# Kernel optimization log

Hardware: AMD Instinct MI355X
Metric: run time of the kernel (lower is better)

Reference implementation:

```python
import jax, jax.numpy as jnp
import numpy as np

N_UE = 100000
N_AP = 10000
N_E = 1600000
D = 64
H = 128


def setup_inputs() -> dict:
    key = jax.random.key(0)
    ks = jax.random.split(key, 10)
    s = 0.05
    return {
        "ue_hid": jax.random.normal(ks[0], (N_UE, D), jnp.float32),
        "ap_hid": jax.random.normal(ks[1], (N_AP, D), jnp.float32),
        "edge_hid": jax.random.normal(ks[2], (N_E, D), jnp.float32),
        "src": jax.random.randint(ks[3], (N_E,), 0, N_UE),
        "dst": jax.random.randint(ks[4], (N_E,), 0, N_AP),
        "W1a": jax.random.normal(ks[5], (2 * D, H), jnp.float32) * s,
        "b1a": jnp.zeros((H,), jnp.float32),
        "W1b": jax.random.normal(ks[6], (H, H), jnp.float32) * s,
        "b1b": jnp.zeros((H,), jnp.float32),
        "W2a": jax.random.normal(ks[7], (D + H, H), jnp.float32) * s,
        "b2a": jnp.zeros((H,), jnp.float32),
        "W2b": jax.random.normal(ks[8], (H, D), jnp.float32) * s,
        "b2b": jnp.zeros((D,), jnp.float32),
    }


def reference(ue_hid, ap_hid, edge_hid, src, dst,
              W1a, b1a, W1b, b1b, W2a, b2a, W2b, b2b):
    # message: concat(edge_feature, src UE feature) -> [E, 2D]
    msg = jnp.concatenate([edge_hid, ue_hid[src]], axis=-1)
    # mlp1 applied per edge (DGL applies it inside reduce on the mailbox,
    # which is equivalent to per-edge application followed by segment sum)
    h = jnp.maximum(msg @ W1a + b1a, 0.0) @ W1b + b1b          # [E, H]
    # sum over mailbox (all edges with the same destination AP)
    agg = jax.ops.segment_sum(h, dst, num_segments=N_AP)        # [N_AP, H]
    # mlp2 on concat(AP hid, aggregated messages)
    z = jnp.concatenate([ap_hid, agg], axis=-1)                 # [N_AP, D+H]
    new_ap = jnp.maximum(z @ W2a + b2a, 0.0) @ W2b + b2b        # [N_AP, D]
    return new_ap
```

## Files before the change

### kernel.cpp

```cpp
#include <hip/hip_runtime.h>
#include <hip/hip_bf16.h>

#define N_UE 100000
#define N_AP 10000
#define N_E  1600000
#define DD   64
#define HH   128
#define NTILE (N_E / 128)

typedef float f32x4 __attribute__((ext_vector_type(4)));
typedef short s8b   __attribute__((ext_vector_type(8)));
typedef short s4b   __attribute__((ext_vector_type(4)));

static __device__ __forceinline__ unsigned short f2bf(float x) {
  union { float f; unsigned int u; } v; v.f = x;
  unsigned int r = v.u + 0x7fffu + ((v.u >> 16) & 1u);
  return (unsigned short)(r >> 16);
}

__global__ void apk0_prep(const float* __restrict__ W1a, short* __restrict__ WTg,
                          int* __restrict__ counts, float* __restrict__ aggW) {
  int i = blockIdx.x * 256 + threadIdx.x;
  int n = gridDim.x * 256;
  for (int x = i; x < 128 * 128; x += n) {
    int col = x >> 7, k = x & 127;
    WTg[x] = (short)f2bf(W1a[k * 128 + col]);
  }
  for (int x = i; x < N_AP; x += n) counts[x] = 0;
  for (int x = i; x < N_AP * 128 / 4; x += n)
    ((float4*)aggW)[x] = make_float4(0.f, 0.f, 0.f, 0.f);
}

__global__ void apk2_hist(const int* __restrict__ dst, int* __restrict__ counts) {
  int i = blockIdx.x * blockDim.x + threadIdx.x;
  int stride = gridDim.x * blockDim.x;
  for (; i < N_E; i += stride) atomicAdd(&counts[dst[i]], 1);
}

__global__ __launch_bounds__(256) void apk3_scan(const int* __restrict__ counts,
                                                 int* __restrict__ offsets,
                                                 int* __restrict__ cursor) {
  __shared__ int p[256];
  int t = threadIdx.x;
  const int CH = 40;
  int start = t * CH, end = min(start + CH, N_AP);
  int s = 0;
  for (int i = start; i < end; i++) s += counts[i];
  p[t] = s;
  __syncthreads();
  for (int d = 1; d < 256; d <<= 1) {
    int v = p[t] + ((t >= d) ? p[t - d] : 0);
    __syncthreads();
    p[t] = v;
    __syncthreads();
  }
  int base = (t == 0) ? 0 : p[t - 1];
  for (int i = start; i < end; i++) {
    offsets[i] = base;
    cursor[i] = base;
    base += counts[i];
  }
  if (t == 255) offsets[N_AP] = base;
}

__global__ void apk4_scatter(const int* __restrict__ dst, const int* __restrict__ src,
                             int* __restrict__ cursor, int4* __restrict__ triple) {
  int i = blockIdx.x * blockDim.x + threadIdx.x;
  int stride = gridDim.x * blockDim.x;
  for (; i < N_E; i += stride) {
    int d = dst[i];
    int pos = atomicAdd(&cursor[d], 1);
    triple[pos] = make_int4(i, src[i], d, 0);
  }
}

__global__ __launch_bounds__(256, 4) void apk5_edges(
    const float* __restrict__ edge_hid, const float* __restrict__ ue_hid,
    const short* __restrict__ WTg, const float* __restrict__ b1a,
    const int4* __restrict__ triple, float* __restrict__ aggW) {
  __shared__ short A[128][132];
  __shared__ int segs[128];
  int t = threadIdx.x;
  int wave = t >> 6, lane = t & 63, quad = lane >> 4, l16 = lane & 15;

  s8b bf[2][4];
  for (int ct = 0; ct < 2; ct++)
    for (int ks = 0; ks < 4; ks++)
      bf[ct][ks] = *(const s8b*)&WTg[(wave * 32 + ct * 16 + l16) * 128 +
                                     ks * 32 + quad * 8];
  float bias0 = b1a[wave * 32 + l16];
  float bias1 = b1a[wave * 32 + 16 + l16];

  int runseg = -1;
  float run0 = 0.f, run1 = 0.f;
  auto flush = [&]() {
    if (runseg >= 0) {
      float f0 = run0 + __shfl_xor(run0, 16); f0 += __shfl_xor(f0, 32);
      float f1 = run1 + __shfl_xor(run1, 16); f1 += __shfl_xor(f1, 32);
      if (quad == 0) {
        atomicAdd(&aggW[(size_t)runseg * 128 + wave * 32 + l16], f0);
        atomicAdd(&aggW[(size_t)runseg * 128 + wave * 32 + 16 + l16], f1);
      }
    }
  };

  const int r = t >> 1, h = t & 1;
  for (int tile = blockIdx.x; tile < NTILE; tile += gridDim.x) {
    int4 tr = triple[(size_t)tile * 128 + r];
    __syncthreads();
    if (h == 0) segs[r] = tr.z;
    {
      const float* srow = h ? (ue_hid + (size_t)tr.y * 64)
                            : (edge_hid + (size_t)tr.x * 64);
      int kb = h * 64;
      #pragma unroll
      for (int cc = 0; cc < 8; cc++) {
        float4 v = ((const float4*)srow)[cc * 2];
        float4 w = ((const float4*)srow)[cc * 2 + 1];
        s8b p;
        p[0] = (short)f2bf(v.x); p[1] = (short)f2bf(v.y);
        p[2] = (short)f2bf(v.z); p[3] = (short)f2bf(v.w);
        p[4] = (short)f2bf(w.x); p[5] = (short)f2bf(w.y);
        p[6] = (short)f2bf(w.z); p[7] = (short)f2bf(w.w);
        *(s8b*)&A[r][kb + cc * 8] = p;
      }
    }
    __syncthreads();

    for (int rt = 0; rt < 8; rt++) {
      s8b a0 = *(const s8b*)&A[rt * 16 + l16][0 + quad * 8];
      s8b a1 = *(const s8b*)&A[rt * 16 + l16][32 + quad * 8];
      s8b a2 = *(const s8b*)&A[rt * 16 + l16][64 + quad * 8];
      s8b a3 = *(const s8b*)&A[rt * 16 + l16][96 + quad * 8];
      f32x4 c0 = {0.f, 0.f, 0.f, 0.f}, c1 = {0.f, 0.f, 0.f, 0.f};
      c0 = __builtin_amdgcn_mfma_f32_16x16x32_bf16(a0, bf[0][0], c0, 0, 0, 0);
      c0 = __builtin_amdgcn_mfma_f32_16x16x32_bf16(a1, bf[0][1], c0, 0, 0, 0);
      c0 = __builtin_amdgcn_mfma_f32_16x16x32_bf16(a2, bf[0][2], c0, 0, 0, 0);
      c0 = __builtin_amdgcn_mfma_f32_16x16x32_bf16(a3, bf[0][3], c0, 0, 0, 0);
      c1 = __builtin_amdgcn_mfma_f32_16x16x32_bf16(a0, bf[1][0], c1, 0, 0, 0);
      c1 = __builtin_amdgcn_mfma_f32_16x16x32_bf16(a1, bf[1][1], c1, 0, 0, 0);
      c1 = __builtin_amdgcn_mfma_f32_16x16x32_bf16(a2, bf[1][2], c1, 0, 0, 0);
      c1 = __builtin_amdgcn_mfma_f32_16x16x32_bf16(a3, bf[1][3], c1, 0, 0, 0);
      float t0[4], t1[4];
      #pragma unroll
      for (int j = 0; j < 4; j++) {
        t0[j] = fmaxf(c0[j] + bias0, 0.f);
        t1[j] = fmaxf(c1[j] + bias1, 0.f);
      }
      int gb = rt * 16;
      int sF = segs[gb], sL = segs[gb + 15];
      if (sF == sL) {
        if (sF != runseg) { flush(); runseg = sF; run0 = 0.f; run1 = 0.f; }
        run0 += t0[0] + t0[1] + t0[2] + t0[3];
        run1 += t1[0] + t1[1] + t1[2] + t1[3];
      } else {
        int sj[4];
        #pragma unroll
        for (int j = 0; j < 4; j++) sj[j] = segs[gb + quad * 4 + j];
        for (int s = sF; s <= sL; s++) {
          float v0 = 0.f, v1 = 0.f;
          #pragma unroll
          for (int j = 0; j < 4; j++)
            if (sj[j] == s) { v0 += t0[j]; v1 += t1[j]; }
          if (s == runseg) { run0 += v0; run1 += v1; }
          else { flush(); runseg = s; run0 = v0; run1 = v1; }
        }
      }
    }
  }
  flush();
}

__global__ __launch_bounds__(256) void apk6_mlp2(
    const float* __restrict__ ap_hid, const float* __restrict__ W1b,
    const float* __restrict__ b1b, const float* __restrict__ W2a,
    const float* __restrict__ b2a, const float* __restrict__ W2b,
    const float* __restrict__ b2b, const float* __restrict__ aggW,
    const int* __restrict__ offsets, float* __restrict__ out) {
  __shared__ float wbuf[64 * 128];
  __shared__ float zrows[16 * 128];
  __shared__ float yrows[16 * 128];
  __shared__ float arows[16 * 64];
  __shared__ float cbuf[16];
  int t = threadIdx.x;
  int apb = blockIdx.x * 16;
  for (int i = t; i < 16 * 128 / 4; i += 256)
    ((float4*)zrows)[i] = ((const float4*)(aggW + (size_t)apb * 128))[i];
  for (int i = t; i < 16 * 64 / 4; i += 256)
    ((float4*)arows)[i] = ((const float4*)(ap_hid + (size_t)apb * 64))[i];
  if (t < 16) cbuf[t] = (float)(offsets[apb + t + 1] - offsets[apb + t]);
  int j = t & 127, half = t >> 7;
  {
    float bb = b1b[j];
    __syncthreads();
    float acc[8];
    for (int r = 0; r < 8; r++) acc[r] = cbuf[half * 8 + r] * bb;
    for (int p = 0; p < 2; p++) {
      __syncthreads();
      for (int i = t; i < 64 * 128 / 4; i += 256)
        ((float4*)wbuf)[i] = ((const float4*)(W1b + p * 64 * 128))[i];
      __syncthreads();
      for (int k = 0; k < 64; k++) {
        float w = wbuf[k * 128 + j];
        for (int r = 0; r < 8; r++)
          acc[r] += zrows[(half * 8 + r) * 128 + (p * 64 + k)] * w;
      }
    }
    for (int r = 0; r < 8; r++) yrows[(half * 8 + r) * 128 + j] = acc[r];
  }
  {
    float acc2[8];
    float bb = b2a[j];
    for (int r = 0; r < 8; r++) acc2[r] = bb;
    __syncthreads();
    for (int i = t; i < 64 * 128 / 4; i += 256)
      ((float4*)wbuf)[i] = ((const float4*)W2a)[i];
    __syncthreads();
    for (int k = 0; k < 64; k++) {
      float w = wbuf[k * 128 + j];
      for (int r = 0; r < 8; r++) acc2[r] += arows[(half * 8 + r) * 64 + k] * w;
    }
    for (int p = 0; p < 2; p++) {
      __syncthreads();
      for (int i = t; i < 64 * 128 / 4; i += 256)
        ((float4*)wbuf)[i] = ((const float4*)(W2a + (64 + p * 64) * 128))[i];
      __syncthreads();
      for (int k = 0; k < 64; k++) {
        float w = wbuf[k * 128 + j];
        for (int r = 0; r < 8; r++)
          acc2[r] += yrows[(half * 8 + r) * 128 + (p * 64 + k)] * w;
      }
    }
    __syncthreads();
    for (int r = 0; r < 8; r++)
      zrows[(half * 8 + r) * 128 + j] = fmaxf(acc2[r], 0.f);
  }
  {
    __syncthreads();
    for (int i = t; i < 128 * 64 / 4; i += 256)
      ((float4*)wbuf)[i] = ((const float4*)W2b)[i];
    __syncthreads();
    int i2 = t & 63, q = t >> 6;
    float acc3[4];
    float bb = b2b[i2];
    for (int r = 0; r < 4; r++) acc3[r] = bb;
    for (int k = 0; k < 128; k++) {
      float w = wbuf[k * 64 + i2];
      for (int r = 0; r < 4; r++) acc3[r] += zrows[(q * 4 + r) * 128 + k] * w;
    }
    for (int r = 0; r < 4; r++)
      out[(size_t)(apb + q * 4 + r) * 64 + i2] = acc3[r];
  }
}

extern "C" void kernel_launch(void* const* d_in, const int* in_sizes, int n_in,
                              void* d_out, int out_size, void* d_ws, size_t ws_size,
                              hipStream_t stream) {
  const float* ue_hid   = (const float*)d_in[0];
  const float* ap_hid   = (const float*)d_in[1];
  const float* edge_hid = (const float*)d_in[2];
  const int*   src      = (const int*)d_in[3];
  const int*   dst      = (const int*)d_in[4];
  const float* W1a      = (const float*)d_in[5];
  const float* b1a      = (const float*)d_in[6];
  const float* W1b      = (const float*)d_in[7];
  const float* b1b      = (const float*)d_in[8];
  const float* W2a      = (const float*)d_in[9];
  const float* b2a      = (const float*)d_in[10];
  const float* W2b      = (const float*)d_in[11];
  const float* b2b      = (const float*)d_in[12];
  float* out = (float*)d_out;

  unsigned char* ws = (unsigned char*)d_ws;
  short* WTg    = (short*)(ws);
  int* counts   = (int*)(ws + 32768);
  int* offsets  = (int*)(ws + 73728);
  int* cursor   = (int*)(ws + 114688);
  float* aggW   = (float*)(ws + 155648);
  int4* triple  = (int4*)(ws + 5275648);

  apk0_prep<<<640, 256, 0, stream>>>(W1a, WTg, counts, aggW);
  apk2_hist<<<2048, 256, 0, stream>>>(dst, counts);
  apk3_scan<<<1, 256, 0, stream>>>(counts, offsets, cursor);
  apk4_scatter<<<2048, 256, 0, stream>>>(dst, src, cursor, triple);
  apk5_edges<<<2048, 256, 0, stream>>>(edge_hid, ue_hid, WTg, b1a, triple, aggW);
  apk6_mlp2<<<N_AP / 16, 256, 0, stream>>>(ap_hid, W1b, b1b, W2a, b2a, W2b, b2b,
                                           aggW, offsets, out);
}
```

Baseline: 917.3 us.

## Fuse preprocessing and edge phases into one cooperative kernel with packed edge records

New measurement: 1.614 ms. 1.76x slower.

```diff
diff --git a/kernel.cpp b/kernel.cpp
--- a/kernel.cpp
+++ b/kernel.cpp
@@ -1,16 +1,17 @@
 #include <hip/hip_runtime.h>
-#include <hip/hip_bf16.h>
+#include <hip/hip_cooperative_groups.h>
+
+namespace cg = cooperative_groups;
 
 #define N_UE 100000
 #define N_AP 10000
 #define N_E  1600000
-#define DD   64
-#define HH   128
 #define NTILE (N_E / 128)
+#define GRID  1024
 
 typedef float f32x4 __attribute__((ext_vector_type(4)));
+typedef int   i32x2 __attribute__((ext_vector_type(2)));
 typedef short s8b   __attribute__((ext_vector_type(8)));
-typedef short s4b   __attribute__((ext_vector_type(4)));
 
 static __device__ __forceinline__ unsigned short f2bf(float x) {
   union { float f; unsigned int u; } v; v.f = x;
@@ -18,68 +19,72 @@
   return (unsigned short)(r >> 16);
 }
 
-__global__ void apk0_prep(const float* __restrict__ W1a, short* __restrict__ WTg,
-                          int* __restrict__ counts, float* __restrict__ aggW) {
-  int i = blockIdx.x * 256 + threadIdx.x;
-  int n = gridDim.x * 256;
+
+static __device__ __forceinline__ void ph0_prep(const float* __restrict__ W1a,
+    short* __restrict__ WTg, int* __restrict__ counts, float* __restrict__ aggW) {
+  int i = blockIdx.x * 256 + threadIdx.x, n = gridDim.x * 256;
   for (int x = i; x < 128 * 128; x += n) {
     int col = x >> 7, k = x & 127;
     WTg[x] = (short)f2bf(W1a[k * 128 + col]);
   }
   for (int x = i; x < N_AP; x += n) counts[x] = 0;
   for (int x = i; x < N_AP * 128 / 4; x += n)
-    ((float4*)aggW)[x] = make_float4(0.f, 0.f, 0.f, 0.f);
-}
-
-__global__ void apk2_hist(const int* __restrict__ dst, int* __restrict__ counts) {
-  int i = blockIdx.x * blockDim.x + threadIdx.x;
-  int stride = gridDim.x * blockDim.x;
-  for (; i < N_E; i += stride) atomicAdd(&counts[dst[i]], 1);
-}
-
-__global__ __launch_bounds__(256) void apk3_scan(const int* __restrict__ counts,
-                                                 int* __restrict__ offsets,
-                                                 int* __restrict__ cursor) {
-  __shared__ int p[256];
-  int t = threadIdx.x;
-  const int CH = 40;
-  int start = t * CH, end = min(start + CH, N_AP);
-  int s = 0;
-  for (int i = start; i < end; i++) s += counts[i];
-  p[t] = s;
+    ((f32x4*)aggW)[x] = (f32x4){0.f, 0.f, 0.f, 0.f};
+}
+
+static __device__ __forceinline__ void ph1_hist(const int* __restrict__ dst,
+                                                int* __restrict__ counts) {
+  int i = blockIdx.x * 256 + threadIdx.x, n = gridDim.x * 256;
+  for (; i < N_E; i += n) atomicAdd(&counts[dst[i]], 1);
+}
+
+static __device__ __forceinline__ void ph2_scanlocal(const int* __restrict__ counts,
+    int* __restrict__ offsets, int* __restrict__ bsum, int* p) {
+  if (blockIdx.x >= 40) return;
+  int t = threadIdx.x, idx = blockIdx.x * 256 + t;
+  int v = (idx < N_AP) ? counts[idx] : 0;
+  p[t] = v;
   __syncthreads();
   for (int d = 1; d < 256; d <<= 1) {
-    int v = p[t] + ((t >= d) ? p[t - d] : 0);
-    __syncthreads();
-    p[t] = v;
-    __syncthreads();
-  }
-  int base = (t == 0) ? 0 : p[t - 1];
-  for (int i = start; i < end; i++) {
-    offsets[i] = base;
-    cursor[i] = base;
-    base += counts[i];
-  }
-  if (t == 255) offsets[N_AP] = base;
-}
-
-__global__ void apk4_scatter(const int* __restrict__ dst, const int* __restrict__ src,
-                             int* __restrict__ cursor, int4* __restrict__ triple) {
-  int i = blockIdx.x * blockDim.x + threadIdx.x;
-  int stride = gridDim.x * blockDim.x;
-  for (; i < N_E; i += stride) {
-    int d = dst[i];
-    int pos = atomicAdd(&cursor[d], 1);
-    triple[pos] = make_int4(i, src[i], d, 0);
-  }
-}
-
-__global__ __launch_bounds__(256, 4) void apk5_edges(
-    const float* __restrict__ edge_hid, const float* __restrict__ ue_hid,
-    const short* __restrict__ WTg, const float* __restrict__ b1a,
-    const int4* __restrict__ triple, float* __restrict__ aggW) {
-  __shared__ short A[128][132];
-  __shared__ int segs[128];
+    int s2 = p[t] + ((t >= d) ? p[t - d] : 0);
+    __syncthreads();
+    p[t] = s2;
+    __syncthreads();
+  }
+  if (idx < N_AP) offsets[idx] = p[t] - v;
+  if (t == 255) bsum[blockIdx.x] = p[255];
+}
+
+static __device__ __forceinline__ void ph3_scanbase(int* __restrict__ offsets,
+    const int* __restrict__ bsum, int* p) {
+  if (blockIdx.x >= 40) return;
+  int t = threadIdx.x, idx = blockIdx.x * 256 + t;
+  if (t == 0) {
+    int b = 0;
+    for (int k = 0; k < (int)blockIdx.x; k++) b += bsum[k];
+    p[0] = b;
+  }
+  __syncthreads();
+  if (idx < N_AP) offsets[idx] += p[0];
+}
+
+static __device__ __forceinline__ void ph4_scatter(const int* __restrict__ dst,
+    const int* __restrict__ src, int* __restrict__ offsets, i32x2* __restrict__ pair) {
+  int i = blockIdx.x * 256 + threadIdx.x, n = gridDim.x * 256;
+  for (; i < N_E; i += n) {
+    int d = dst[i], s = src[i];
+    int pos = atomicAdd(&offsets[d], 1);
+    i32x2 v;
+    v[0] = i | ((d & 0x7FF) << 21);
+    v[1] = s | ((d >> 11) << 17);
+    __builtin_nontemporal_store(v, &pair[pos]);
+  }
+}
+
+static __device__ void ph5_edges(const float* __restrict__ edge_hid,
+    const float* __restrict__ ue_hid, const short* __restrict__ WTg,
+    const float* __restrict__ b1a, const i32x2* __restrict__ pair,
+    float* __restrict__ aggW, short (*A)[132], int* segs) {
   int t = threadIdx.x;
   int wave = t >> 6, lane = t & 63, quad = lane >> 4, l16 = lane & 15;
 
@@ -106,23 +111,37 @@
 
   const int r = t >> 1, h = t & 1;
   for (int tile = blockIdx.x; tile < NTILE; tile += gridDim.x) {
-    int4 tr = triple[(size_t)tile * 128 + r];
-    __syncthreads();
-    if (h == 0) segs[r] = tr.z;
-    {
-      const float* srow = h ? (ue_hid + (size_t)tr.y * 64)
-                            : (edge_hid + (size_t)tr.x * 64);
-      int kb = h * 64;
+    i32x2 tr = __builtin_nontemporal_load(&pair[(size_t)tile * 128 + r]);
+    int e = tr[0] & 0x1FFFFF;
+    int d = (int)((unsigned)tr[0] >> 21) | (((tr[1] >> 17) & 7) << 11);
+    int s = tr[1] & 0x1FFFF;
+    __syncthreads();
+    if (h == 0) {
+      segs[r] = d;
+      const f32x4* s4 = (const f32x4*)(edge_hid + (size_t)e * 64);
       #pragma unroll
       for (int cc = 0; cc < 8; cc++) {
-        float4 v = ((const float4*)srow)[cc * 2];
-        float4 w = ((const float4*)srow)[cc * 2 + 1];
-        s8b p;
-        p[0] = (short)f2bf(v.x); p[1] = (short)f2bf(v.y);
-        p[2] = (short)f2bf(v.z); p[3] = (short)f2bf(v.w);
-        p[4] = (short)f2bf(w.x); p[5] = (short)f2bf(w.y);
-        p[6] = (short)f2bf(w.z); p[7] = (short)f2bf(w.w);
-        *(s8b*)&A[r][kb + cc * 8] = p;
+        f32x4 v = __builtin_nontemporal_load(&s4[cc * 2]);
+        f32x4 w = __builtin_nontemporal_load(&s4[cc * 2 + 1]);
+        s8b pk;
+        pk[0] = (short)f2bf(v[0]); pk[1] = (short)f2bf(v[1]);
+        pk[2] = (short)f2bf(v[2]); pk[3] = (short)f2bf(v[3]);
+        pk[4] = (short)f2bf(w[0]); pk[5] = (short)f2bf(w[1]);
+        pk[6] = (short)f2bf(w[2]); pk[7] = (short)f2bf(w[3]);
+        *(s8b*)&A[r][cc * 8] = pk;
+      }
+    } else {
+      const f32x4* s4 = (const f32x4*)(ue_hid + (size_t)s * 64);
+      #pragma unroll
+      for (int cc = 0; cc < 8; cc++) {
+        f32x4 v = s4[cc * 2];
+        f32x4 w = s4[cc * 2 + 1];
+        s8b pk;
+        pk[0] = (short)f2bf(v[0]); pk[1] = (short)f2bf(v[1]);
+        pk[2] = (short)f2bf(v[2]); pk[3] = (short)f2bf(v[3]);
+        pk[4] = (short)f2bf(w[0]); pk[5] = (short)f2bf(w[1]);
+        pk[6] = (short)f2bf(w[2]); pk[7] = (short)f2bf(w[3]);
+        *(s8b*)&A[r][64 + cc * 8] = pk;
       }
     }
     __syncthreads();
@@ -157,18 +176,56 @@
         int sj[4];
         #pragma unroll
         for (int j = 0; j < 4; j++) sj[j] = segs[gb + quad * 4 + j];
-        for (int s = sF; s <= sL; s++) {
+        for (int sg = sF; sg <= sL; sg++) {
           float v0 = 0.f, v1 = 0.f;
           #pragma unroll
           for (int j = 0; j < 4; j++)
-            if (sj[j] == s) { v0 += t0[j]; v1 += t1[j]; }
-          if (s == runseg) { run0 += v0; run1 += v1; }
-          else { flush(); runseg = s; run0 = v0; run1 = v1; }
+            if (sj[j] == sg) { v0 += t0[j]; v1 += t1[j]; }
+          if (sg == runseg) { run0 += v0; run1 += v1; }
+          else { flush(); runseg = sg; run0 = v0; run1 = v1; }
         }
       }
     }
   }
   flush();
+}
+
+
+__global__ __launch_bounds__(256, 4) void apc_all(
+    const float* __restrict__ W1a, const float* __restrict__ b1a,
+    const float* __restrict__ edge_hid, const float* __restrict__ ue_hid,
+    const int* __restrict__ src, const int* __restrict__ dst,
+    short* __restrict__ WTg, int* __restrict__ counts, int* __restrict__ offsets,
+    int* __restrict__ bsum, i32x2* __restrict__ pair, float* __restrict__ aggW) {
+  __shared__ short A[128][132];
+  __shared__ int segs[128];
+  __shared__ int p[256];
+  cg::grid_group g = cg::this_grid();
+  ph0_prep(W1a, WTg, counts, aggW);          g.sync();
+  ph1_hist(dst, counts);                     g.sync();
+  ph2_scanlocal(counts, offsets, bsum, p);   g.sync();
+  ph3_scanbase(offsets, bsum, p);            g.sync();
+  ph4_scatter(dst, src, offsets, pair);      g.sync();
+  ph5_edges(edge_hid, ue_hid, WTg, b1a, pair, aggW, A, segs);
+}
+
+__global__ __launch_bounds__(256, 4) void apc_one(int phase,
+    const float* __restrict__ W1a, const float* __restrict__ b1a,
+    const float* __restrict__ edge_hid, const float* __restrict__ ue_hid,
+    const int* __restrict__ src, const int* __restrict__ dst,
+    short* __restrict__ WTg, int* __restrict__ counts, int* __restrict__ offsets,
+    int* __restrict__ bsum, i32x2* __restrict__ pair, float* __restrict__ aggW) {
+  __shared__ short A[128][132];
+  __shared__ int segs[128];
+  __shared__ int p[256];
+  switch (phase) {
+    case 0: ph0_prep(W1a, WTg, counts, aggW); break;
+    case 1: ph1_hist(dst, counts); break;
+    case 2: ph2_scanlocal(counts, offsets, bsum, p); break;
+    case 3: ph3_scanbase(offsets, bsum, p); break;
+    case 4: ph4_scatter(dst, src, offsets, pair); break;
+    case 5: ph5_edges(edge_hid, ue_hid, WTg, b1a, pair, aggW, A, segs); break;
+  }
 }
 
 __global__ __launch_bounds__(256) void apk6_mlp2(
@@ -176,7 +233,7 @@
     const float* __restrict__ b1b, const float* __restrict__ W2a,
     const float* __restrict__ b2a, const float* __restrict__ W2b,
     const float* __restrict__ b2b, const float* __restrict__ aggW,
-    const int* __restrict__ offsets, float* __restrict__ out) {
+    const int* __restrict__ counts, float* __restrict__ out) {
   __shared__ float wbuf[64 * 128];
   __shared__ float zrows[16 * 128];
   __shared__ float yrows[16 * 128];
@@ -188,22 +245,22 @@
     ((float4*)zrows)[i] = ((const float4*)(aggW + (size_t)apb * 128))[i];
   for (int i = t; i < 16 * 64 / 4; i += 256)
     ((float4*)arows)[i] = ((const float4*)(ap_hid + (size_t)apb * 64))[i];
-  if (t < 16) cbuf[t] = (float)(offsets[apb + t + 1] - offsets[apb + t]);
+  if (t < 16) cbuf[t] = (float)counts[apb + t];
   int j = t & 127, half = t >> 7;
   {
     float bb = b1b[j];
     __syncthreads();
     float acc[8];
     for (int r = 0; r < 8; r++) acc[r] = cbuf[half * 8 + r] * bb;
-    for (int p = 0; p < 2; p++) {
+    for (int pp = 0; pp < 2; pp++) {
       __syncthreads();
       for (int i = t; i < 64 * 128 / 4; i += 256)
-        ((float4*)wbuf)[i] = ((const float4*)(W1b + p * 64 * 128))[i];
+        ((float4*)wbuf)[i] = ((const float4*)(W1b + pp * 64 * 128))[i];
       __syncthreads();
       for (int k = 0; k < 64; k++) {
         float w = wbuf[k * 128 + j];
         for (int r = 0; r < 8; r++)
-          acc[r] += zrows[(half * 8 + r) * 128 + (p * 64 + k)] * w;
+          acc[r] += zrows[(half * 8 + r) * 128 + (pp * 64 + k)] * w;
       }
     }
     for (int r = 0; r < 8; r++) yrows[(half * 8 + r) * 128 + j] = acc[r];
@@ -220,15 +277,15 @@
       float w = wbuf[k * 128 + j];
       for (int r = 0; r < 8; r++) acc2[r] += arows[(half * 8 + r) * 64 + k] * w;
     }
-    for (int p = 0; p < 2; p++) {
+    for (int pp = 0; pp < 2; pp++) {
       __syncthreads();
       for (int i = t; i < 64 * 128 / 4; i += 256)
-        ((float4*)wbuf)[i] = ((const float4*)(W2a + (64 + p * 64) * 128))[i];
+        ((float4*)wbuf)[i] = ((const float4*)(W2a + (64 + pp * 64) * 128))[i];
       __syncthreads();
       for (int k = 0; k < 64; k++) {
         float w = wbuf[k * 128 + j];
         for (int r = 0; r < 8; r++)
-          acc2[r] += yrows[(half * 8 + r) * 128 + (p * 64 + k)] * w;
+          acc2[r] += yrows[(half * 8 + r) * 128 + (pp * 64 + k)] * w;
       }
     }
     __syncthreads();
@@ -275,15 +332,20 @@
   short* WTg    = (short*)(ws);
   int* counts   = (int*)(ws + 32768);
   int* offsets  = (int*)(ws + 73728);
-  int* cursor   = (int*)(ws + 114688);
-  float* aggW   = (float*)(ws + 155648);
-  int4* triple  = (int4*)(ws + 5275648);
-
-  apk0_prep<<<640, 256, 0, stream>>>(W1a, WTg, counts, aggW);
-  apk2_hist<<<2048, 256, 0, stream>>>(dst, counts);
-  apk3_scan<<<1, 256, 0, stream>>>(counts, offsets, cursor);
-  apk4_scatter<<<2048, 256, 0, stream>>>(dst, src, cursor, triple);
-  apk5_edges<<<2048, 256, 0, stream>>>(edge_hid, ue_hid, WTg, b1a, triple, aggW);
+  int* bsum     = (int*)(ws + 114688);
+  float* aggW   = (float*)(ws + 118784);
+  i32x2* pair   = (i32x2*)(ws + 5238784);
+
+  void* args[] = {(void*)&W1a, (void*)&b1a, (void*)&edge_hid, (void*)&ue_hid,
+                  (void*)&src, (void*)&dst, (void*)&WTg, (void*)&counts,
+                  (void*)&offsets, (void*)&bsum, (void*)&pair, (void*)&aggW};
+  hipError_t cerr = hipLaunchCooperativeKernel((void*)apc_all, dim3(GRID), dim3(256),
+                                               args, 0, stream);
+  if (cerr != hipSuccess) {
+    for (int p = 0; p < 6; p++)
+      apc_one<<<GRID, 256, 0, stream>>>(p, W1a, b1a, edge_hid, ue_hid, src, dst,
+                                        WTg, counts, offsets, bsum, pair, aggW);
+  }
   apk6_mlp2<<<N_AP / 16, 256, 0, stream>>>(ap_hid, W1b, b1b, W2a, b2a, W2b, b2b,
-                                           aggW, offsets, out);
-}
+                                           aggW, counts, out);
+}
```

## Pack edge triples into 8-byte pairs, parallelize scan, coalesce row gathers

Applied to the files above, without the earlier changes.

Result: faster. 829.0 us (-9.6%).

```diff
diff --git a/kernel.cpp b/kernel.cpp
--- a/kernel.cpp
+++ b/kernel.cpp
@@ -1,14 +1,12 @@
 #include <hip/hip_runtime.h>
-#include <hip/hip_bf16.h>
 
 #define N_UE 100000
 #define N_AP 10000
 #define N_E  1600000
-#define DD   64
-#define HH   128
 #define NTILE (N_E / 128)
 
 typedef float f32x4 __attribute__((ext_vector_type(4)));
+typedef int   i32x2 __attribute__((ext_vector_type(2)));
 typedef short s8b   __attribute__((ext_vector_type(8)));
 typedef short s4b   __attribute__((ext_vector_type(4)));
 
@@ -20,15 +18,14 @@
 
 __global__ void apk0_prep(const float* __restrict__ W1a, short* __restrict__ WTg,
                           int* __restrict__ counts, float* __restrict__ aggW) {
-  int i = blockIdx.x * 256 + threadIdx.x;
-  int n = gridDim.x * 256;
+  int i = blockIdx.x * 256 + threadIdx.x, n = gridDim.x * 256;
   for (int x = i; x < 128 * 128; x += n) {
     int col = x >> 7, k = x & 127;
     WTg[x] = (short)f2bf(W1a[k * 128 + col]);
   }
   for (int x = i; x < N_AP; x += n) counts[x] = 0;
   for (int x = i; x < N_AP * 128 / 4; x += n)
-    ((float4*)aggW)[x] = make_float4(0.f, 0.f, 0.f, 0.f);
+    ((f32x4*)aggW)[x] = (f32x4){0.f, 0.f, 0.f, 0.f};
 }
 
 __global__ void apk2_hist(const int* __restrict__ dst, int* __restrict__ counts) {
@@ -37,49 +34,59 @@
   for (; i < N_E; i += stride) atomicAdd(&counts[dst[i]], 1);
 }
 
-__global__ __launch_bounds__(256) void apk3_scan(const int* __restrict__ counts,
-                                                 int* __restrict__ offsets,
-                                                 int* __restrict__ cursor) {
+__global__ __launch_bounds__(256) void apk3a_scanlocal(
+    const int* __restrict__ counts, int* __restrict__ offsets,
+    int* __restrict__ bsum) {
   __shared__ int p[256];
-  int t = threadIdx.x;
-  const int CH = 40;
-  int start = t * CH, end = min(start + CH, N_AP);
-  int s = 0;
-  for (int i = start; i < end; i++) s += counts[i];
-  p[t] = s;
+  int t = threadIdx.x, idx = blockIdx.x * 256 + t;
+  int v = (idx < N_AP) ? counts[idx] : 0;
+  p[t] = v;
   __syncthreads();
   for (int d = 1; d < 256; d <<= 1) {
-    int v = p[t] + ((t >= d) ? p[t - d] : 0);
-    __syncthreads();
-    p[t] = v;
-    __syncthreads();
-  }
-  int base = (t == 0) ? 0 : p[t - 1];
-  for (int i = start; i < end; i++) {
-    offsets[i] = base;
-    cursor[i] = base;
-    base += counts[i];
-  }
-  if (t == 255) offsets[N_AP] = base;
+    int s2 = p[t] + ((t >= d) ? p[t - d] : 0);
+    __syncthreads();
+    p[t] = s2;
+    __syncthreads();
+  }
+  if (idx < N_AP) offsets[idx] = p[t] - v;
+  if (t == 255) bsum[blockIdx.x] = p[255];
+}
+
+__global__ __launch_bounds__(256) void apk3b_scanbase(
+    int* __restrict__ offsets, const int* __restrict__ bsum) {
+  __shared__ int base;
+  int t = threadIdx.x, idx = blockIdx.x * 256 + t;
+  if (t == 0) {
+    int b = 0;
+    for (int k = 0; k < (int)blockIdx.x; k++) b += bsum[k];
+    base = b;
+  }
+  __syncthreads();
+  if (idx < N_AP) offsets[idx] += base;
 }
 
 __global__ void apk4_scatter(const int* __restrict__ dst, const int* __restrict__ src,
-                             int* __restrict__ cursor, int4* __restrict__ triple) {
+                             int* __restrict__ offsets, i32x2* __restrict__ pair) {
   int i = blockIdx.x * blockDim.x + threadIdx.x;
   int stride = gridDim.x * blockDim.x;
   for (; i < N_E; i += stride) {
-    int d = dst[i];
-    int pos = atomicAdd(&cursor[d], 1);
-    triple[pos] = make_int4(i, src[i], d, 0);
+    int d = dst[i], s = src[i];
+    int pos = atomicAdd(&offsets[d], 1);
+    i32x2 v;
+    v[0] = i | ((d & 0x7FF) << 21);
+    v[1] = s | ((d >> 11) << 17);
+    pair[pos] = v;
   }
 }
 
 __global__ __launch_bounds__(256, 4) void apk5_edges(
     const float* __restrict__ edge_hid, const float* __restrict__ ue_hid,
     const short* __restrict__ WTg, const float* __restrict__ b1a,
-    const int4* __restrict__ triple, float* __restrict__ aggW) {
+    const i32x2* __restrict__ pair, float* __restrict__ aggW) {
   __shared__ short A[128][132];
   __shared__ int segs[128];
+  __shared__ int eix[128];
+  __shared__ int six[128];
   int t = threadIdx.x;
   int wave = t >> 6, lane = t & 63, quad = lane >> 4, l16 = lane & 15;
 
@@ -104,25 +111,32 @@
     }
   };
 
-  const int r = t >> 1, h = t & 1;
+  const int r8 = t >> 5, half = (t >> 4) & 1, chunk = t & 15;
   for (int tile = blockIdx.x; tile < NTILE; tile += gridDim.x) {
-    int4 tr = triple[(size_t)tile * 128 + r];
-    __syncthreads();
-    if (h == 0) segs[r] = tr.z;
+    __syncthreads();
+    if (t < 128) {
+      i32x2 tr = pair[(size_t)tile * 128 + t];
+      segs[t] = (int)((unsigned)tr[0] >> 21) | (((tr[1] >> 17) & 7) << 11);
+      eix[t] = tr[0] & 0x1FFFFF;
+      six[t] = tr[1] & 0x1FFFF;
+    }
+    __syncthreads();
     {
-      const float* srow = h ? (ue_hid + (size_t)tr.y * 64)
-                            : (edge_hid + (size_t)tr.x * 64);
-      int kb = h * 64;
+      const float* bases[16];
       #pragma unroll
-      for (int cc = 0; cc < 8; cc++) {
-        float4 v = ((const float4*)srow)[cc * 2];
-        float4 w = ((const float4*)srow)[cc * 2 + 1];
-        s8b p;
-        p[0] = (short)f2bf(v.x); p[1] = (short)f2bf(v.y);
-        p[2] = (short)f2bf(v.z); p[3] = (short)f2bf(v.w);
-        p[4] = (short)f2bf(w.x); p[5] = (short)f2bf(w.y);
-        p[6] = (short)f2bf(w.z); p[7] = (short)f2bf(w.w);
-        *(s8b*)&A[r][kb + cc * 8] = p;
+      for (int it = 0; it < 16; it++) {
+        int row = it * 8 + r8;
+        bases[it] = half ? (ue_hid + (size_t)six[row] * 64)
+                         : (edge_hid + (size_t)eix[row] * 64);
+      }
+      #pragma unroll
+      for (int it = 0; it < 16; it++) {
+        int row = it * 8 + r8;
+        f32x4 v = ((const f32x4*)bases[it])[chunk];
+        s4b pk;
+        pk[0] = (short)f2bf(v[0]); pk[1] = (short)f2bf(v[1]);
+        pk[2] = (short)f2bf(v[2]); pk[3] = (short)f2bf(v[3]);
+        *(s4b*)&A[row][half * 64 + chunk * 4] = pk;
       }
     }
     __syncthreads();
@@ -157,13 +171,13 @@
         int sj[4];
         #pragma unroll
         for (int j = 0; j < 4; j++) sj[j] = segs[gb + quad * 4 + j];
-        for (int s = sF; s <= sL; s++) {
+        for (int sg = sF; sg <= sL; sg++) {
           float v0 = 0.f, v1 = 0.f;
           #pragma unroll
           for (int j = 0; j < 4; j++)
-            if (sj[j] == s) { v0 += t0[j]; v1 += t1[j]; }
-          if (s == runseg) { run0 += v0; run1 += v1; }
-          else { flush(); runseg = s; run0 = v0; run1 = v1; }
+            if (sj[j] == sg) { v0 += t0[j]; v1 += t1[j]; }
+          if (sg == runseg) { run0 += v0; run1 += v1; }
+          else { flush(); runseg = sg; run0 = v0; run1 = v1; }
         }
       }
     }
@@ -176,7 +190,7 @@
     const float* __restrict__ b1b, const float* __restrict__ W2a,
     const float* __restrict__ b2a, const float* __restrict__ W2b,
     const float* __restrict__ b2b, const float* __restrict__ aggW,
-    const int* __restrict__ offsets, float* __restrict__ out) {
+    const int* __restrict__ counts, float* __restrict__ out) {
   __shared__ float wbuf[64 * 128];
   __shared__ float zrows[16 * 128];
   __shared__ float yrows[16 * 128];
@@ -188,22 +202,22 @@
     ((float4*)zrows)[i] = ((const float4*)(aggW + (size_t)apb * 128))[i];
   for (int i = t; i < 16 * 64 / 4; i += 256)
     ((float4*)arows)[i] = ((const float4*)(ap_hid + (size_t)apb * 64))[i];
-  if (t < 16) cbuf[t] = (float)(offsets[apb + t + 1] - offsets[apb + t]);
+  if (t < 16) cbuf[t] = (float)counts[apb + t];
   int j = t & 127, half = t >> 7;
   {
     float bb = b1b[j];
     __syncthreads();
     float acc[8];
     for (int r = 0; r < 8; r++) acc[r] = cbuf[half * 8 + r] * bb;
-    for (int p = 0; p < 2; p++) {
+    for (int pp = 0; pp < 2; pp++) {
       __syncthreads();
       for (int i = t; i < 64 * 128 / 4; i += 256)
-        ((float4*)wbuf)[i] = ((const float4*)(W1b + p * 64 * 128))[i];
+        ((float4*)wbuf)[i] = ((const float4*)(W1b + pp * 64 * 128))[i];
       __syncthreads();
       for (int k = 0; k < 64; k++) {
         float w = wbuf[k * 128 + j];
         for (int r = 0; r < 8; r++)
-          acc[r] += zrows[(half * 8 + r) * 128 + (p * 64 + k)] * w;
+          acc[r] += zrows[(half * 8 + r) * 128 + (pp * 64 + k)] * w;
       }
     }
     for (int r = 0; r < 8; r++) yrows[(half * 8 + r) * 128 + j] = acc[r];
@@ -220,15 +234,15 @@
       float w = wbuf[k * 128 + j];
       for (int r = 0; r < 8; r++) acc2[r] += arows[(half * 8 + r) * 64 + k] * w;
     }
-    for (int p = 0; p < 2; p++) {
+    for (int pp = 0; pp < 2; pp++) {
       __syncthreads();
       for (int i = t; i < 64 * 128 / 4; i += 256)
-        ((float4*)wbuf)[i] = ((const float4*)(W2a + (64 + p * 64) * 128))[i];
+        ((float4*)wbuf)[i] = ((const float4*)(W2a + (64 + pp * 64) * 128))[i];
       __syncthreads();
       for (int k = 0; k < 64; k++) {
         float w = wbuf[k * 128 + j];
         for (int r = 0; r < 8; r++)
-          acc2[r] += yrows[(half * 8 + r) * 128 + (p * 64 + k)] * w;
+          acc2[r] += yrows[(half * 8 + r) * 128 + (pp * 64 + k)] * w;
       }
     }
     __syncthreads();
@@ -275,15 +289,16 @@
   short* WTg    = (short*)(ws);
   int* counts   = (int*)(ws + 32768);
   int* offsets  = (int*)(ws + 73728);
-  int* cursor   = (int*)(ws + 114688);
-  float* aggW   = (float*)(ws + 155648);
-  int4* triple  = (int4*)(ws + 5275648);
+  int* bsum     = (int*)(ws + 114688);
+  float* aggW   = (float*)(ws + 118784);
+  i32x2* pair   = (i32x2*)(ws + 5238784);
 
   apk0_prep<<<640, 256, 0, stream>>>(W1a, WTg, counts, aggW);
   apk2_hist<<<2048, 256, 0, stream>>>(dst, counts);
-  apk3_scan<<<1, 256, 0, stream>>>(counts, offsets, cursor);
-  apk4_scatter<<<2048, 256, 0, stream>>>(dst, src, cursor, triple);
-  apk5_edges<<<2048, 256, 0, stream>>>(edge_hid, ue_hid, WTg, b1a, triple, aggW);
+  apk3a_scanlocal<<<40, 256, 0, stream>>>(counts, offsets, bsum);
+  apk3b_scanbase<<<40, 256, 0, stream>>>(offsets, bsum);
+  apk4_scatter<<<2048, 256, 0, stream>>>(dst, src, offsets, pair);
+  apk5_edges<<<2048, 256, 0, stream>>>(edge_hid, ue_hid, WTg, b1a, pair, aggW);
   apk6_mlp2<<<N_AP / 16, 256, 0, stream>>>(ap_hid, W1b, b1b, W2a, b2a, W2b, b2b,
-                                           aggW, offsets, out);
-}
+                                           aggW, counts, out);
+}
```
